# Optimization experiments

Measured on AMD Instinct MI355X. Metric: run time of the kernel, lower is better.

## Reference

```python
import jax, jax.numpy as jnp
import numpy as np

N_NODES = 50000
N_EDGES = 1600000
IN_CH = 32
HID = 64
K = 2


def _dconv(X, edge_index, edge_weight, W, b):
    """Diffusion graph conv (torch_geometric_temporal DConv, K=2).

    X: [N, C_in], W: [2, K, C_in, C_out], b: [C_out].
    Direction 0: forward transition P_f = D_out^{-1} A  (applied as P_f^T X).
    Direction 1: backward transition P_b = D_in^{-1} A^T (applied as P_b^T X).
    """
    n = X.shape[0]
    row, col = edge_index[0], edge_index[1]
    deg_out = jax.ops.segment_sum(edge_weight, row, num_segments=n)  # out-degree (row sums of A)
    deg_in = jax.ops.segment_sum(edge_weight, col, num_segments=n)   # in-degree  (col sums of A)
    norm_out = edge_weight / deg_out[row]  # [E]
    norm_in = edge_weight / deg_in[col]    # [E]

    # k = 0 term: identity for both directions
    H = X @ (W[0, 0] + W[1, 0])

    # k = 1 term: one diffusion step in each direction
    # forward dir: out[i] = sum_{(j->i)} w/deg_out[j] * X[j]
    Tx_o = jax.ops.segment_sum(norm_out[:, None] * X[row], col, num_segments=n)
    # backward dir: out[i] = sum_{(i->j)} w/deg_in[j] * X[j]
    Tx_i = jax.ops.segment_sum(norm_in[:, None] * X[col], row, num_segments=n)
    H = H + Tx_o @ W[0, 1] + Tx_i @ W[1, 1]
    return H + b


def setup_inputs() -> dict:
    key = jax.random.key(0)
    ks = jax.random.split(key, 12)
    cat_ch = IN_CH + HID  # GRU concatenates [X, H]
    s = 1.0 / np.sqrt(cat_ch)
    inp = {
        "x": jax.random.normal(ks[0], (N_NODES, IN_CH), dtype=jnp.float32),
        "edge_index": jax.random.randint(ks[1], (2, N_EDGES), 0, N_NODES, dtype=jnp.int32),
        "edge_weight": jax.random.uniform(ks[2], (N_EDGES,), dtype=jnp.float32, minval=0.05, maxval=1.0),
        "Wz": jax.random.uniform(ks[3], (2, K, cat_ch, HID), dtype=jnp.float32, minval=-s, maxval=s),
        "bz": jnp.zeros((HID,), dtype=jnp.float32),
        "Wr": jax.random.uniform(ks[4], (2, K, cat_ch, HID), dtype=jnp.float32, minval=-s, maxval=s),
        "br": jnp.zeros((HID,), dtype=jnp.float32),
        "Wh": jax.random.uniform(ks[5], (2, K, cat_ch, HID), dtype=jnp.float32, minval=-s, maxval=s),
        "bh": jnp.zeros((HID,), dtype=jnp.float32),
        "Wlin": jax.random.uniform(ks[6], (HID, 1), dtype=jnp.float32, minval=-1.0 / np.sqrt(HID), maxval=1.0 / np.sqrt(HID)),
        "blin": jnp.zeros((1,), dtype=jnp.float32),
    }
    return inp


def reference(x, edge_index, edge_weight, Wz, bz, Wr, br, Wh, bh, Wlin, blin):
    n = x.shape[0]
    H0 = jnp.zeros((n, HID), dtype=x.dtype)  # initial hidden state (H=None)
    XH = jnp.concatenate([x, H0], axis=-1)   # [N, IN_CH+HID]
    Z = jax.nn.sigmoid(_dconv(XH, edge_index, edge_weight, Wz, bz))
    R = jax.nn.sigmoid(_dconv(XH, edge_index, edge_weight, Wr, br))
    XHR = jnp.concatenate([x, H0 * R], axis=-1)
    H_tilde = jnp.tanh(_dconv(XHR, edge_index, edge_weight, Wh, bh))
    H = Z * H0 + (1.0 - Z) * H_tilde
    out = jnp.maximum(H, 0.0) @ Wlin + blin  # ReLU then Linear(hidden, 1)
    return out
```

## Files before the change

kernel.cpp:

```cpp
#include <hip/hip_runtime.h>
#include <math.h>

#define N_NODES 50000
#define N_EDGES 1600000
#define IN_CH 32
#define HID 64

#define NBIN 782
#define BIN_SHIFT 6
#define CHUNK 8192
#define NCHK ((N_EDGES + CHUNK - 1) / CHUNK)
#define CNTG_N (2 * NBIN * NCHK)
#define CNTG_N4 (CNTG_N / 4)
#define SCAN_BLOCKS ((CNTG_N4 + 1023) / 1024)
#define FG_CAP 2560

#define PREP_WPREP_BLOCKS 48
#define PREP_XCONV_BLOCKS ((N_NODES * 8 + 255) / 256)
#define PREP_BLOCKS (NCHK + PREP_WPREP_BLOCKS + PREP_XCONV_BLOCKS)

#define WS_RDEG_OUT 0
#define WS_RDEG_IN  50000
#define WS_CNTG     100000
#define WS_BLKSUM   406548
#define WS_WBF      406676
#define WS_BINCNT   412820
#define WS_XSB      512916
#define WS_TXO      1312916
#define WS_TXI      2112916
#define WS_BINNED   2912916
#define WS_END      9312916

typedef __attribute__((ext_vector_type(8))) short bf16x8;
typedef __attribute__((ext_vector_type(4))) float f32x4;

__device__ __forceinline__ unsigned short f2bf(float f) {
    unsigned int u = __float_as_uint(f);
    return (unsigned short)((u + 0x7fffu + ((u >> 16) & 1u)) >> 16);
}
__device__ __forceinline__ float bf2f(unsigned short b) {
    return __uint_as_float((unsigned int)b << 16);
}

__global__ __launch_bounds__(256) void prep_kernel(
    const int* __restrict__ ei, const float* __restrict__ Wz,
    const float* __restrict__ Wh, const float4* __restrict__ x4,
    int* __restrict__ cntG, unsigned short* __restrict__ wbf,
    ushort4* __restrict__ xsb) {
    __shared__ int h[2 * NBIN];
    int tid = threadIdx.x;
    int b = blockIdx.x;
    if (b < NCHK) {
        for (int i = tid; i < 2 * NBIN; i += 256) h[i] = 0;
        __syncthreads();
        int e0 = b * CHUNK;
        int e1 = min(e0 + CHUNK, N_EDGES);
        for (int e = e0 + tid; e < e1; e += 256) {
            int r = ei[e];
            int c = ei[N_EDGES + e];
            atomicAdd(&h[c >> BIN_SHIFT], 1);
            atomicAdd(&h[NBIN + (r >> BIN_SHIFT)], 1);
        }
        __syncthreads();
        for (int i = tid; i < 2 * NBIN; i += 256) cntG[i * NCHK + b] = h[i];
    } else if (b < NCHK + PREP_WPREP_BLOCKS) {
        int idx = (b - NCHK) * 256 + tid;
        if (idx >= 12288) return;
        int j = idx & 7, ln = (idx >> 3) & 63, bn = (idx >> 9) & 7, kk = idx >> 12;
        int k = kk * 32 + (ln >> 4) * 8 + j;
        int n = bn * 16 + (ln & 15);
        int slab = k >> 5, c = k & 31;
        const float* W = (n < 64) ? Wz : Wh;
        int o = n & 63;
        float v;
        if (slab == 0)      v = W[c * 64 + o] + W[(2 * 96 + c) * 64 + o];
        else if (slab == 1) v = W[(96 + c) * 64 + o];
        else                v = W[(3 * 96 + c) * 64 + o];
        wbf[idx] = f2bf(v);
    } else {
        int i = (b - NCHK - PREP_WPREP_BLOCKS) * 256 + tid;
        if (i >= N_NODES * 8) return;
        float4 v = x4[i];
        ushort4 o;
        o.x = f2bf(v.x); o.y = f2bf(v.y); o.z = f2bf(v.z); o.w = f2bf(v.w);
        xsb[i] = o;
    }
}

__global__ __launch_bounds__(256) void scan_partial_kernel(
    const int4* __restrict__ cnt4, int* __restrict__ blksum, int n4) {
    __shared__ int s[256];
    int t = threadIdx.x;
    int base4 = blockIdx.x * 1024 + t * 4;
    int total = 0;
#pragma unroll
    for (int j = 0; j < 4; ++j) {
        int idx = base4 + j;
        if (idx < n4) {
            int4 v = cnt4[idx];
            total += v.x + v.y + v.z + v.w;
        }
    }
    s[t] = total;
    __syncthreads();
    for (int off = 128; off > 0; off >>= 1) {
        if (t < off) s[t] += s[t + off];
        __syncthreads();
    }
    if (t == 0) blksum[blockIdx.x] = s[0];
}

__global__ __launch_bounds__(256) void scan_blocksum_kernel(int* __restrict__ blksum, int nb) {
    __shared__ int s[256];
    int t = threadIdx.x;
    int v = (t < nb) ? blksum[t] : 0;
    s[t] = v;
    __syncthreads();
    for (int off = 1; off < 256; off <<= 1) {
        int u = (t >= off) ? s[t - off] : 0;
        __syncthreads();
        s[t] += u;
        __syncthreads();
    }
    if (t < nb) blksum[t] = s[t] - v;
}

__global__ __launch_bounds__(256) void scan_final_kernel(
    int4* __restrict__ cnt4, const int* __restrict__ blksum, int n4) {
    __shared__ int s[256];
    int t = threadIdx.x;
    int base4 = blockIdx.x * 1024 + t * 4;
    int4 vals[4];
    int total = 0;
#pragma unroll
    for (int j = 0; j < 4; ++j) {
        int idx = base4 + j;
        vals[j] = (idx < n4) ? cnt4[idx] : make_int4(0, 0, 0, 0);
        total += vals[j].x + vals[j].y + vals[j].z + vals[j].w;
    }
    s[t] = total;
    __syncthreads();
    for (int off = 1; off < 256; off <<= 1) {
        int u = (t >= off) ? s[t - off] : 0;
        __syncthreads();
        s[t] += u;
        __syncthreads();
    }
    int run = blksum[blockIdx.x] + s[t] - total;
#pragma unroll
    for (int j = 0; j < 4; ++j) {
        int idx = base4 + j;
        int4 v = vals[j];
        int4 o;
        o.x = run; run += v.x;
        o.y = run; run += v.y;
        o.z = run; run += v.z;
        o.w = run; run += v.w;
        if (idx < n4) cnt4[idx] = o;
    }
}

__global__ __launch_bounds__(512) void partition_kernel(
    const int* __restrict__ ei, const float* __restrict__ ew,
    const int* __restrict__ cntG, int2* __restrict__ binned) {
    __shared__ int2 stg[CHUNK];
    __shared__ int hist[NBIN];
    __shared__ int lst[NBIN];
    __shared__ int gStart[NBIN];
    __shared__ int sc[512];
    int tid = threadIdx.x;
    int dir = (blockIdx.x >= NCHK) ? 1 : 0;
    int chunk = blockIdx.x - dir * NCHK;

    for (int i = tid; i < NBIN; i += 512) hist[i] = 0;
    __syncthreads();

    int e0 = chunk * CHUNK;
    int n_e = min(CHUNK, N_EDGES - e0);
    int binv[16], rankv[16];
    int2 pay[16];
#pragma unroll
    for (int j = 0; j < 16; ++j) {
        int idx = tid + j * 512;
        if (idx < n_e) {
            int e = e0 + idx;
            int r = ei[e];
            int c = ei[N_EDGES + e];
            int dst = dir ? r : c;
            int src = dir ? c : r;
            int b = dst >> BIN_SHIFT;
            binv[j] = b;
            rankv[j] = atomicAdd(&hist[b], 1);
            pay[j] = make_int2((int)(((unsigned)b << 22) | ((unsigned)(dst & 63) << 16) |
                                     (unsigned)src),
                               __float_as_int(ew[e]));
        } else {
            binv[j] = -1;
        }
    }
    __syncthreads();
    int ps = (tid < 391) ? (hist[2 * tid] + hist[2 * tid + 1]) : 0;
    sc[tid] = ps;
    __syncthreads();
    for (int off = 1; off < 512; off <<= 1) {
        int u = (tid >= off) ? sc[tid - off] : 0;
        __syncthreads();
        sc[tid] += u;
        __syncthreads();
    }
    if (tid < 391) {
        int pref = sc[tid] - ps;
        lst[2 * tid] = pref;
        lst[2 * tid + 1] = pref + hist[2 * tid];
    }
    for (int i = tid; i < NBIN; i += 512)
        gStart[i] = cntG[(dir * NBIN + i) * NCHK + chunk];
    __syncthreads();
#pragma unroll
    for (int j = 0; j < 16; ++j)
        if (binv[j] >= 0) stg[lst[binv[j]] + rankv[j]] = pay[j];
    __syncthreads();
    for (int p = tid; p < n_e; p += 512) {
        int2 v2 = stg[p];
        int b = (int)(((unsigned)v2.x) >> 22);
        int gpos = gStart[b] + (p - lst[b]);
        binned[gpos] = make_int2(v2.x & 0x3FFFFF, v2.y);
    }
}

__device__ __forceinline__ void bin_range(const int* cntG, int b, int& lo, int& hi) {
    lo = cntG[b * NCHK];
    hi = (b + 1 < 2 * NBIN) ? cntG[(b + 1) * NCHK] : 2 * N_EDGES;
}

__global__ __launch_bounds__(256) void bindeg_kernel(
    const int* __restrict__ cntG, const int2* __restrict__ binned,
    int* __restrict__ binCnt, float* __restrict__ ws_f) {
    __shared__ float wsum[64];
    __shared__ int cnt[64];
    int tid = threadIdx.x;
    int b = blockIdx.x;
    int dir = (b >= NBIN) ? 1 : 0;
    if (tid < 64) { wsum[tid] = 0.f; cnt[tid] = 0; }
    __syncthreads();
    int lo, hi;
    bin_range(cntG, b, lo, hi);
    for (int p = lo + tid; p < hi; p += 256) {
        int2 v = binned[p];
        int d = v.x >> 16;
        atomicAdd(&cnt[d], 1);
        atomicAdd(&wsum[d], __int_as_float(v.y));
    }
    __syncthreads();
    if (tid < 64) {
        binCnt[b * 64 + tid] = cnt[tid];
        int node = (b - dir * NBIN) * 64 + tid;
        if (node < N_NODES) {
            float s = wsum[tid];
            float* rdeg = ws_f + (dir == 0 ? WS_RDEG_IN : WS_RDEG_OUT);
            rdeg[node] = (s != 0.f) ? (1.f / s) : 0.f;
        }
    }
}

__global__ __launch_bounds__(256) void fgather_kernel(
    const ushort4* __restrict__ xsb, const int* __restrict__ cntG,
    const int* __restrict__ binCnt, const int2* __restrict__ binned,
    float* __restrict__ ws_f) {
    __shared__ int2 s_edge[FG_CAP];
    __shared__ int s_off[65];
    __shared__ int s_cur[64];
    __shared__ int sc[64];
    int tid = threadIdx.x;
    int b = blockIdx.x;
    int dir = (b >= NBIN) ? 1 : 0;
    int bin = b - dir * NBIN;

    int v = (tid < 64) ? binCnt[b * 64 + tid] : 0;
    if (tid < 64) sc[tid] = v;
    __syncthreads();
    for (int off = 1; off < 64; off <<= 1) {
        int u = (tid < 64 && tid >= off) ? sc[tid - off] : 0;
        __syncthreads();
        if (tid < 64) sc[tid] += u;
        __syncthreads();
    }
    if (tid < 64) {
        s_off[tid] = sc[tid] - v;
        s_cur[tid] = sc[tid] - v;
    }
    if (tid == 63) s_off[64] = sc[63];
    __syncthreads();

    const float* rdeg = ws_f + (dir == 0 ? WS_RDEG_OUT : WS_RDEG_IN);
    int lo, hi;
    bin_range(cntG, b, lo, hi);
    int n_e = hi - lo;
    for (int p = tid; p < n_e; p += 256) {
        int2 ev = binned[lo + p];
        int src = ev.x & 0xffff;
        float coef = __int_as_float(ev.y) * rdeg[src];
        int rk = atomicAdd(&s_cur[ev.x >> 16], 1);
        if (rk < FG_CAP) s_edge[rk] = make_int2(src, __float_as_int(coef));
    }
    __syncthreads();

    ushort4* outp = (ushort4*)(ws_f + (dir == 0 ? WS_TXO : WS_TXI));
    int lane = tid & 7;
#pragma unroll
    for (int it = 0; it < 2; ++it) {
        int nl = it * 32 + (tid >> 3);
        int p = s_off[nl], end = s_off[nl + 1];
        float4 acc = make_float4(0.f, 0.f, 0.f, 0.f);
        for (; p + 3 < end; p += 4) {
            int2 v0 = s_edge[p], v1 = s_edge[p + 1];
            int2 v2 = s_edge[p + 2], v3 = s_edge[p + 3];
            ushort4 a0 = xsb[v0.x * 8 + lane];
            ushort4 a1 = xsb[v1.x * 8 + lane];
            ushort4 a2 = xsb[v2.x * 8 + lane];
            ushort4 a3 = xsb[v3.x * 8 + lane];
            float c0 = __int_as_float(v0.y), c1 = __int_as_float(v1.y);
            float c2 = __int_as_float(v2.y), c3 = __int_as_float(v3.y);
            acc.x += c0 * bf2f(a0.x) + c1 * bf2f(a1.x) + c2 * bf2f(a2.x) + c3 * bf2f(a3.x);
            acc.y += c0 * bf2f(a0.y) + c1 * bf2f(a1.y) + c2 * bf2f(a2.y) + c3 * bf2f(a3.y);
            acc.z += c0 * bf2f(a0.z) + c1 * bf2f(a1.z) + c2 * bf2f(a2.z) + c3 * bf2f(a3.z);
            acc.w += c0 * bf2f(a0.w) + c1 * bf2f(a1.w) + c2 * bf2f(a2.w) + c3 * bf2f(a3.w);
        }
        for (; p < end; ++p) {
            int2 v0 = s_edge[p];
            float c0 = __int_as_float(v0.y);
            ushort4 a = xsb[v0.x * 8 + lane];
            acc.x += c0 * bf2f(a.x);
            acc.y += c0 * bf2f(a.y);
            acc.z += c0 * bf2f(a.z);
            acc.w += c0 * bf2f(a.w);
        }
        int node = bin * 64 + nl;
        if (node < N_NODES) {
            ushort4 o;
            o.x = f2bf(acc.x); o.y = f2bf(acc.y);
            o.z = f2bf(acc.z); o.w = f2bf(acc.w);
            outp[node * 8 + lane] = o;
        }
    }
}

#define DN_GROUP 64
#define DN_BLOCKS ((N_NODES + DN_GROUP - 1) / DN_GROUP)
__global__ __launch_bounds__(256) void dense_kernel(
    const int4* __restrict__ xsb4,
    const int4* __restrict__ txo_b, const int4* __restrict__ txi_b,
    const unsigned short* __restrict__ wbf,
    const float* __restrict__ bz, const float* __restrict__ bh,
    const float* __restrict__ Wlin, const float* __restrict__ blin,
    float* __restrict__ out) {
    __shared__ unsigned short sA[64 * 104];
    __shared__ unsigned short sB[12288];

    int tid = threadIdx.x;
    int lane = tid & 63, w = tid >> 6;
    int lm = lane & 15, quad = lane >> 4;

    for (int idx = tid; idx < 3072; idx += 256)
        *(ushort4*)&sB[idx * 4] = ((const ushort4*)wbf)[idx];

    int node0 = blockIdx.x * DN_GROUP;
    for (int idx = tid; idx < 64 * 4; idx += 256) {
        int nl = idx >> 2, q = idx & 3;
        int node = node0 + nl;
        int4 v = (node < N_NODES) ? xsb4[node * 4 + q] : make_int4(0, 0, 0, 0);
        *(int4*)&sA[nl * 104 + q * 8] = v;
    }
    for (int idx = tid; idx < 64 * 8; idx += 256) {
        int nl = idx >> 3, q = idx & 7;
        int node = node0 + nl;
        int4 v = make_int4(0, 0, 0, 0);
        if (node < N_NODES)
            v = (q < 4) ? txo_b[node * 4 + q] : txi_b[node * 4 + (q - 4)];
        *(int4*)&sA[nl * 104 + 32 + q * 8] = v;
    }

    float bzv[4], bhv[4], wlv[4];
#pragma unroll
    for (int bn = 0; bn < 4; ++bn) {
        int o = lm + 16 * bn;
        bzv[bn] = bz[o]; bhv[bn] = bh[o]; wlv[bn] = Wlin[o];
    }
    float bl = blin[0];
    __syncthreads();

    f32x4 acc[8];
#pragma unroll
    for (int bn = 0; bn < 4; ++bn) {
        acc[bn]     = (f32x4){bzv[bn], bzv[bn], bzv[bn], bzv[bn]};
        acc[bn + 4] = (f32x4){bhv[bn], bhv[bn], bhv[bn], bhv[bn]};
    }
#pragma unroll
    for (int kk = 0; kk < 3; ++kk) {
        bf16x8 af = *(const bf16x8*)&sA[(w * 16 + lm) * 104 + kk * 32 + quad * 8];
#pragma unroll
        for (int bn = 0; bn < 8; ++bn) {
            bf16x8 bf = *(const bf16x8*)&sB[((kk * 8 + bn) * 64 + lane) * 8];
            acc[bn] = __builtin_amdgcn_mfma_f32_16x16x32_bf16(af, bf, acc[bn], 0, 0, 0);
        }
    }

    float partial[4] = {0.f, 0.f, 0.f, 0.f};
#pragma unroll
    for (int bn = 0; bn < 4; ++bn) {
#pragma unroll
        for (int reg = 0; reg < 4; ++reg) {
            float az = acc[bn][reg], ah = acc[bn + 4][reg];
            float z = 1.f / (1.f + __expf(-az));
            float ht = 1.f - 2.f / (__expf(2.f * ah) + 1.f);
            partial[reg] += fmaxf((1.f - z) * ht, 0.f) * wlv[bn];
        }
    }
#pragma unroll
    for (int reg = 0; reg < 4; ++reg) {
        float s = partial[reg];
        s += __shfl_xor(s, 1, 64);
        s += __shfl_xor(s, 2, 64);
        s += __shfl_xor(s, 4, 64);
        s += __shfl_xor(s, 8, 64);
        if (lm == 0) {
            int node = node0 + w * 16 + quad * 4 + reg;
            if (node < N_NODES) out[node] = s + bl;
        }
    }
}

extern "C" void kernel_launch(void* const* d_in, const int* in_sizes, int n_in,
                              void* d_out, int out_size, void* d_ws, size_t ws_size,
                              hipStream_t stream) {
    const float* x = (const float*)d_in[0];
    const int* ei = (const int*)d_in[1];
    const float* ew = (const float*)d_in[2];
    const float* Wz = (const float*)d_in[3];
    const float* bz = (const float*)d_in[4];
    const float* Wh = (const float*)d_in[7];
    const float* bh = (const float*)d_in[8];
    const float* Wlin = (const float*)d_in[9];
    const float* blin = (const float*)d_in[10];
    float* out = (float*)d_out;
    float* wf = (float*)d_ws;
    int* wi = (int*)d_ws;
    int2* binned = (int2*)(wi + WS_BINNED);

    prep_kernel<<<PREP_BLOCKS, 256, 0, stream>>>(
        ei, Wz, Wh, (const float4*)x, wi + WS_CNTG,
        (unsigned short*)(wi + WS_WBF), (ushort4*)(wi + WS_XSB));
    scan_partial_kernel<<<SCAN_BLOCKS, 256, 0, stream>>>(
        (const int4*)(wi + WS_CNTG), wi + WS_BLKSUM, CNTG_N4);
    scan_blocksum_kernel<<<1, 256, 0, stream>>>(wi + WS_BLKSUM, SCAN_BLOCKS);
    scan_final_kernel<<<SCAN_BLOCKS, 256, 0, stream>>>(
        (int4*)(wi + WS_CNTG), wi + WS_BLKSUM, CNTG_N4);
    partition_kernel<<<2 * NCHK, 512, 0, stream>>>(ei, ew, wi + WS_CNTG, binned);
    bindeg_kernel<<<2 * NBIN, 256, 0, stream>>>(
        wi + WS_CNTG, binned, wi + WS_BINCNT, wf);
    fgather_kernel<<<2 * NBIN, 256, 0, stream>>>(
        (const ushort4*)(wi + WS_XSB), wi + WS_CNTG, wi + WS_BINCNT, binned, wf);
    dense_kernel<<<DN_BLOCKS, 256, 0, stream>>>(
        (const int4*)(wi + WS_XSB), (const int4*)(wi + WS_TXO),
        (const int4*)(wi + WS_TXI), (const unsigned short*)(wi + WS_WBF),
        bz, bh, Wlin, blin, out);
}
```

Before: 196.0 us.

## Replace per-node edge sort in fgather with shared-memory atomic accumulation

```diff
diff --git a/kernel.cpp b/kernel.cpp
--- a/kernel.cpp
+++ b/kernel.cpp
@@ -13,7 +13,6 @@
 #define CNTG_N (2 * NBIN * NCHK)
 #define CNTG_N4 (CNTG_N / 4)
 #define SCAN_BLOCKS ((CNTG_N4 + 1023) / 1024)
-#define FG_CAP 2560
 
 #define PREP_WPREP_BLOCKS 48
 #define PREP_XCONV_BLOCKS ((N_NODES * 8 + 255) / 256)
@@ -24,12 +23,11 @@
 #define WS_CNTG     100000
 #define WS_BLKSUM   406548
 #define WS_WBF      406676
-#define WS_BINCNT   412820
-#define WS_XSB      512916
-#define WS_TXO      1312916
-#define WS_TXI      2112916
-#define WS_BINNED   2912916
-#define WS_END      9312916
+#define WS_XSB      412820
+#define WS_TXO      1212820
+#define WS_TXI      2012820
+#define WS_BINNED   2812820
+#define WS_END      9212820
 
 typedef __attribute__((ext_vector_type(8))) short bf16x8;
 typedef __attribute__((ext_vector_type(4))) float f32x4;
@@ -235,25 +233,21 @@
 
 __global__ __launch_bounds__(256) void bindeg_kernel(
     const int* __restrict__ cntG, const int2* __restrict__ binned,
-    int* __restrict__ binCnt, float* __restrict__ ws_f) {
+    float* __restrict__ ws_f) {
     __shared__ float wsum[64];
-    __shared__ int cnt[64];
     int tid = threadIdx.x;
     int b = blockIdx.x;
     int dir = (b >= NBIN) ? 1 : 0;
-    if (tid < 64) { wsum[tid] = 0.f; cnt[tid] = 0; }
+    if (tid < 64) wsum[tid] = 0.f;
     __syncthreads();
     int lo, hi;
     bin_range(cntG, b, lo, hi);
     for (int p = lo + tid; p < hi; p += 256) {
         int2 v = binned[p];
-        int d = v.x >> 16;
-        atomicAdd(&cnt[d], 1);
-        atomicAdd(&wsum[d], __int_as_float(v.y));
+        atomicAdd(&wsum[v.x >> 16], __int_as_float(v.y));
     }
     __syncthreads();
     if (tid < 64) {
-        binCnt[b * 64 + tid] = cnt[tid];
         int node = (b - dir * NBIN) * 64 + tid;
         if (node < N_NODES) {
             float s = wsum[tid];
@@ -263,84 +257,66 @@
     }
 }
 
+#define FG_STRIDE 33
 __global__ __launch_bounds__(256) void fgather_kernel(
     const ushort4* __restrict__ xsb, const int* __restrict__ cntG,
-    const int* __restrict__ binCnt, const int2* __restrict__ binned,
-    float* __restrict__ ws_f) {
-    __shared__ int2 s_edge[FG_CAP];
-    __shared__ int s_off[65];
-    __shared__ int s_cur[64];
-    __shared__ int sc[64];
+    const int2* __restrict__ binned, float* __restrict__ ws_f) {
+    __shared__ float s_acc[64 * FG_STRIDE];
     int tid = threadIdx.x;
     int b = blockIdx.x;
     int dir = (b >= NBIN) ? 1 : 0;
     int bin = b - dir * NBIN;
-
-    int v = (tid < 64) ? binCnt[b * 64 + tid] : 0;
-    if (tid < 64) sc[tid] = v;
-    __syncthreads();
-    for (int off = 1; off < 64; off <<= 1) {
-        int u = (tid < 64 && tid >= off) ? sc[tid - off] : 0;
-        __syncthreads();
-        if (tid < 64) sc[tid] += u;
-        __syncthreads();
-    }
-    if (tid < 64) {
-        s_off[tid] = sc[tid] - v;
-        s_cur[tid] = sc[tid] - v;
-    }
-    if (tid == 63) s_off[64] = sc[63];
-    __syncthreads();
-
+    for (int i = tid; i < 64 * FG_STRIDE; i += 256) s_acc[i] = 0.f;
     const float* rdeg = ws_f + (dir == 0 ? WS_RDEG_OUT : WS_RDEG_IN);
+    __syncthreads();
+
     int lo, hi;
     bin_range(cntG, b, lo, hi);
-    int n_e = hi - lo;
-    for (int p = tid; p < n_e; p += 256) {
-        int2 ev = binned[lo + p];
-        int src = ev.x & 0xffff;
-        float coef = __int_as_float(ev.y) * rdeg[src];
-        int rk = atomicAdd(&s_cur[ev.x >> 16], 1);
-        if (rk < FG_CAP) s_edge[rk] = make_int2(src, __float_as_int(coef));
+    int lane = tid & 7;
+    int slot = tid >> 3;
+    int p = lo + slot;
+    for (; p + 32 < hi; p += 64) {
+        int2 e0 = binned[p];
+        int2 e1 = binned[p + 32];
+        int s0 = e0.x & 0xffff, s1 = e1.x & 0xffff;
+        ushort4 a0 = xsb[s0 * 8 + lane];
+        ushort4 a1 = xsb[s1 * 8 + lane];
+        float c0 = __int_as_float(e0.y) * rdeg[s0];
+        float c1 = __int_as_float(e1.y) * rdeg[s1];
+        float* q0 = &s_acc[(e0.x >> 16) * FG_STRIDE + lane * 4];
+        float* q1 = &s_acc[(e1.x >> 16) * FG_STRIDE + lane * 4];
+        atomicAdd(&q0[0], c0 * bf2f(a0.x));
+        atomicAdd(&q0[1], c0 * bf2f(a0.y));
+        atomicAdd(&q0[2], c0 * bf2f(a0.z));
+        atomicAdd(&q0[3], c0 * bf2f(a0.w));
+        atomicAdd(&q1[0], c1 * bf2f(a1.x));
+        atomicAdd(&q1[1], c1 * bf2f(a1.y));
+        atomicAdd(&q1[2], c1 * bf2f(a1.z));
+        atomicAdd(&q1[3], c1 * bf2f(a1.w));
+    }
+    if (p < hi) {
+        int2 e0 = binned[p];
+        int s0 = e0.x & 0xffff;
+        ushort4 a0 = xsb[s0 * 8 + lane];
+        float c0 = __int_as_float(e0.y) * rdeg[s0];
+        float* q0 = &s_acc[(e0.x >> 16) * FG_STRIDE + lane * 4];
+        atomicAdd(&q0[0], c0 * bf2f(a0.x));
+        atomicAdd(&q0[1], c0 * bf2f(a0.y));
+        atomicAdd(&q0[2], c0 * bf2f(a0.z));
+        atomicAdd(&q0[3], c0 * bf2f(a0.w));
     }
     __syncthreads();
 
     ushort4* outp = (ushort4*)(ws_f + (dir == 0 ? WS_TXO : WS_TXI));
-    int lane = tid & 7;
-#pragma unroll
-    for (int it = 0; it < 2; ++it) {
-        int nl = it * 32 + (tid >> 3);
-        int p = s_off[nl], end = s_off[nl + 1];
-        float4 acc = make_float4(0.f, 0.f, 0.f, 0.f);
-        for (; p + 3 < end; p += 4) {
-            int2 v0 = s_edge[p], v1 = s_edge[p + 1];
-            int2 v2 = s_edge[p + 2], v3 = s_edge[p + 3];
-            ushort4 a0 = xsb[v0.x * 8 + lane];
-            ushort4 a1 = xsb[v1.x * 8 + lane];
-            ushort4 a2 = xsb[v2.x * 8 + lane];
-            ushort4 a3 = xsb[v3.x * 8 + lane];
-            float c0 = __int_as_float(v0.y), c1 = __int_as_float(v1.y);
-            float c2 = __int_as_float(v2.y), c3 = __int_as_float(v3.y);
-            acc.x += c0 * bf2f(a0.x) + c1 * bf2f(a1.x) + c2 * bf2f(a2.x) + c3 * bf2f(a3.x);
-            acc.y += c0 * bf2f(a0.y) + c1 * bf2f(a1.y) + c2 * bf2f(a2.y) + c3 * bf2f(a3.y);
-            acc.z += c0 * bf2f(a0.z) + c1 * bf2f(a1.z) + c2 * bf2f(a2.z) + c3 * bf2f(a3.z);
-            acc.w += c0 * bf2f(a0.w) + c1 * bf2f(a1.w) + c2 * bf2f(a2.w) + c3 * bf2f(a3.w);
-        }
-        for (; p < end; ++p) {
-            int2 v0 = s_edge[p];
-            float c0 = __int_as_float(v0.y);
-            ushort4 a = xsb[v0.x * 8 + lane];
-            acc.x += c0 * bf2f(a.x);
-            acc.y += c0 * bf2f(a.y);
-            acc.z += c0 * bf2f(a.z);
-            acc.w += c0 * bf2f(a.w);
-        }
+    for (int idx = tid; idx < 64 * 8; idx += 256) {
+        int nl = idx >> 3, q = idx & 7;
         int node = bin * 64 + nl;
         if (node < N_NODES) {
+            const float* ap = &s_acc[nl * FG_STRIDE + q * 4];
             ushort4 o;
-            o.x = f2bf(acc.x); o.y = f2bf(acc.y);
-            o.z = f2bf(acc.z); o.w = f2bf(acc.w);
-            outp[node * 8 + lane] = o;
+            o.x = f2bf(ap[0]); o.y = f2bf(ap[1]);
+            o.z = f2bf(ap[2]); o.w = f2bf(ap[3]);
+            outp[node * 8 + q] = o;
         }
     }
 }
@@ -456,10 +432,9 @@
     scan_final_kernel<<<SCAN_BLOCKS, 256, 0, stream>>>(
         (int4*)(wi + WS_CNTG), wi + WS_BLKSUM, CNTG_N4);
     partition_kernel<<<2 * NCHK, 512, 0, stream>>>(ei, ew, wi + WS_CNTG, binned);
-    bindeg_kernel<<<2 * NBIN, 256, 0, stream>>>(
-        wi + WS_CNTG, binned, wi + WS_BINCNT, wf);
+    bindeg_kernel<<<2 * NBIN, 256, 0, stream>>>(wi + WS_CNTG, binned, wf);
     fgather_kernel<<<2 * NBIN, 256, 0, stream>>>(
-        (const ushort4*)(wi + WS_XSB), wi + WS_CNTG, wi + WS_BINCNT, binned, wf);
+        (const ushort4*)(wi + WS_XSB), wi + WS_CNTG, binned, wf);
     dense_kernel<<<DN_BLOCKS, 256, 0, stream>>>(
         (const int4*)(wi + WS_XSB), (const int4*)(wi + WS_TXO),
         (const int4*)(wi + WS_TXI), (const unsigned short*)(wi + WS_WBF),
```

New measurement: 746.6 us. 3.81x slower.
